# Optimization experiments

Measured on AMD Instinct MI355X. Metric: run time of the kernel, lower is better.

Reference implementation:

```python
import jax, jax.numpy as jnp
import numpy as np

N_NODES = 100000
N_EDGES = 1600000
IN_C = 128
HID_C = 128
OUT_C = 64
N_GRAPHS = 64


def setup_inputs() -> dict:
    key = jax.random.key(0)
    ks = jax.random.split(key, 12)
    x = jax.random.normal(ks[0], (N_NODES, IN_C), dtype=jnp.float32)
    edge_index = jax.random.randint(ks[1], (2, N_EDGES), 0, N_NODES, dtype=jnp.int64)
    batch = jnp.sort(jax.random.randint(ks[2], (N_NODES,), 0, N_GRAPHS, dtype=jnp.int64))
    def glorot(k, fan_in, fan_out):
        s = jnp.sqrt(6.0 / (fan_in + fan_out))
        return jax.random.uniform(k, (fan_in, fan_out), jnp.float32, -s, s)
    W1 = glorot(ks[3], IN_C, HID_C);  b1 = jnp.zeros((HID_C,), jnp.float32)
    W2 = glorot(ks[4], HID_C, HID_C); b2 = jnp.zeros((HID_C,), jnp.float32)
    W3 = glorot(ks[5], HID_C, HID_C); b3 = jnp.zeros((HID_C,), jnp.float32)
    Wlin = glorot(ks[6], HID_C, OUT_C)
    blin = jnp.zeros((OUT_C,), jnp.float32)
    return {"x": x, "edge_index": edge_index, "batch": batch,
            "W1": W1, "b1": b1, "W2": W2, "b2": b2, "W3": W3, "b3": b3,
            "Wlin": Wlin, "blin": blin}


def _gcn_conv(x, W, b, src, dst, norm):
    # PyG GCNConv: h = x @ W; out[dst] += norm * h[src]; out += b
    h = x @ W
    msg = h[src] * norm[:, None]                     # [E+N, C] edge-wise gather (memory-bound)
    out = jax.ops.segment_sum(msg, dst, num_segments=N_NODES)
    return out + b


def reference(x, edge_index, batch, W1, b1, W2, b2, W3, b3, Wlin, blin):
    # add self-loops (PyG default add_self_loops=True)
    loops = jnp.arange(N_NODES, dtype=edge_index.dtype)
    src = jnp.concatenate([edge_index[0], loops])
    dst = jnp.concatenate([edge_index[1], loops])
    # symmetric normalization: deg over dst with unit edge weights
    deg = jax.ops.segment_sum(jnp.ones_like(src, dtype=x.dtype), dst, num_segments=N_NODES)
    dinv = jnp.where(deg > 0, jax.lax.rsqrt(deg), 0.0)
    norm = dinv[src] * dinv[dst]                     # [E+N]

    h = jax.nn.relu(_gcn_conv(x, W1, b1, src, dst, norm))
    h = jax.nn.relu(_gcn_conv(h, W2, b2, src, dst, norm))
    h = jax.nn.relu(_gcn_conv(h, W3, b3, src, dst, norm))

    # global mean pool over graphs
    sums = jax.ops.segment_sum(h, batch, num_segments=N_GRAPHS)
    cnts = jax.ops.segment_sum(jnp.ones((N_NODES,), h.dtype), batch, num_segments=N_GRAPHS)
    pooled = sums / jnp.clip(cnts, 1.0)[:, None]     # [G, HID_C]
    return pooled @ Wlin + blin                      # [G, OUT_C]
```

## Files before the change

kernel.cpp:

```cpp
#include <hip/hip_runtime.h>
#include <stdint.h>

#define C_HID 128
#define NGRAPH 64
#define COUT 64
#define POOL_S 64
#define NBLK 256
#define BKT 256
#define NBUK_MAX 512
#define SCAN_CH 4096

typedef short bf16x8 __attribute__((ext_vector_type(8)));
typedef float f32x4 __attribute__((ext_vector_type(4)));
typedef float f32x2 __attribute__((ext_vector_type(2)));

__device__ __forceinline__ unsigned short f2bf(float f){
  unsigned int u = __builtin_bit_cast(unsigned int, f);
  u = u + 0x7FFFu + ((u >> 16) & 1u);
  return (unsigned short)(u >> 16);
}
__device__ __forceinline__ float bflo(unsigned int u){
  return __builtin_bit_cast(float, u << 16);
}
__device__ __forceinline__ float bfhi(unsigned int u){
  return __builtin_bit_cast(float, u & 0xFFFF0000u);
}
__device__ __forceinline__ int clampi(int v, int lo, int hi){
  return v < lo ? lo : (v > hi ? hi : v);
}

__global__ void k_zero(float* __restrict__ out, int n){
  int i = blockIdx.x*blockDim.x + threadIdx.x;
  if (i < n) out[i] = 0.f;
}

__global__ __launch_bounds__(256) void k_cnt(const int* __restrict__ dst,
                                             int* __restrict__ cntg,
                                             int E, int N, int NBUK, int chunk){
  __shared__ int cnt[NBUK_MAX];
  int blk = blockIdx.x, t = threadIdx.x;
  for (int b = t; b < NBUK; b += 256) cnt[b] = 0;
  __syncthreads();
  int e0 = blk*chunk, e1 = min(E, e0 + chunk);
  for (int e = e0 + t; e < e1; e += 256)
    atomicAdd(&cnt[clampi(dst[e], 0, N-1) >> 8], 1);
  __syncthreads();
  for (int b = t; b < NBUK; b += 256)
    cntg[b*NBLK + blk] = cnt[b];
}

__global__ __launch_bounds__(256) void k_scanA(const int* __restrict__ cnt,
                                               int* __restrict__ bsum, int n){
  __shared__ int red[256];
  int blk = blockIdx.x, t = threadIdx.x;
  int base = blk*SCAN_CH + t*16;
  int s = 0;
  #pragma unroll
  for (int j = 0; j < 16; ++j){ int i = base + j; s += (i < n) ? cnt[i] : 0; }
  red[t] = s; __syncthreads();
  for (int off = 128; off > 0; off >>= 1){
    if (t < off) red[t] += red[t + off];
    __syncthreads();
  }
  if (t == 0) bsum[blk] = red[0];
}

__global__ __launch_bounds__(256) void k_scanB(const int* __restrict__ bsum,
                                               int* __restrict__ bbase,
                                               int* __restrict__ bases, int nb, int n){
  __shared__ int buf[256];
  int t = threadIdx.x;
  int v = (t < nb) ? bsum[t] : 0;
  buf[t] = v; __syncthreads();
  for (int off = 1; off < 256; off <<= 1){
    int add = (t >= off) ? buf[t-off] : 0;
    __syncthreads();
    buf[t] += add;
    __syncthreads();
  }
  if (t < nb) bbase[t] = buf[t] - v;
  if (t == nb-1) bases[n] = buf[t];
}

__global__ __launch_bounds__(256) void k_scanC(const int* __restrict__ cnt,
                                               const int* __restrict__ bbase,
                                               int* __restrict__ bases, int n){
  __shared__ int buf[256];
  int blk = blockIdx.x, t = threadIdx.x;
  int base = blk*SCAN_CH + t*16;
  int loc[16]; int s = 0;
  #pragma unroll
  for (int j = 0; j < 16; ++j){ int i = base + j; loc[j] = (i < n) ? cnt[i] : 0; s += loc[j]; }
  buf[t] = s; __syncthreads();
  for (int off = 1; off < 256; off <<= 1){
    int add = (t >= off) ? buf[t-off] : 0;
    __syncthreads();
    buf[t] += add;
    __syncthreads();
  }
  int run = bbase[blk] + buf[t] - s;
  #pragma unroll
  for (int j = 0; j < 16; ++j){
    int i = base + j;
    if (i < n) bases[i] = run;
    run += loc[j];
  }
}

__global__ __launch_bounds__(256) void k_scat(const int* __restrict__ src,
                                              const int* __restrict__ dst,
                                              const int* __restrict__ bases,
                                              unsigned int* __restrict__ rec,
                                              int E, int N, int NBUK, int chunk){
  __shared__ int cur[NBUK_MAX];
  int blk = blockIdx.x, t = threadIdx.x;
  for (int b = t; b < NBUK; b += 256) cur[b] = bases[b*NBLK + blk];
  __syncthreads();
  int e0 = blk*chunk, e1 = min(E, e0 + chunk);
  for (int e = e0 + t; e < e1; e += 256){
    int d = clampi(dst[e], 0, N-1);
    int s = clampi(src[e], 0, N-1);
    int p = atomicAdd(&cur[d >> 8], 1);
    rec[p] = (unsigned int)s | ((unsigned int)(d & 255) << 24);
  }
}

__global__ __launch_bounds__(256) void k_csr(const unsigned int* __restrict__ rec,
                                             const int* __restrict__ bases,
                                             int* __restrict__ offs, float* __restrict__ dinv,
                                             int* __restrict__ meta, int E, int N, int NBUK){
  __shared__ int cnt[BKT], loff[BKT], cur[BKT];
  int b = blockIdx.x, t = threadIdx.x;
  cnt[t] = 0;
  __syncthreads();
  int r0 = bases[b*NBLK];
  int r1 = (b+1 < NBUK) ? bases[(b+1)*NBLK] : E;
  for (int i = r0 + t; i < r1; i += 256)
    atomicAdd(&cnt[rec[i] >> 24], 1);
  __syncthreads();
  loff[t] = cnt[t];
  __syncthreads();
  for (int off = 1; off < BKT; off <<= 1){
    int add = (t >= off) ? loff[t - off] : 0;
    __syncthreads();
    loff[t] += add;
    __syncthreads();
  }
  int excl = loff[t] - cnt[t];
  cur[t] = r0 + excl;
  int node = b*BKT + t;
  if (node < N){
    offs[node] = r0 + excl;
    dinv[node] = rsqrtf((float)(cnt[t] + 1));
  }
  if (b == NBUK-1 && t == 0) offs[N] = E;
  __syncthreads();
  for (int i = r0 + t; i < r1; i += 256){
    unsigned int r = rec[i];
    int p = atomicAdd(&cur[r >> 24], 1);
    meta[p] = (int)(r & 0x00FFFFFFu);
  }
}

__global__ void k_xcast(const float2* __restrict__ x, const float* __restrict__ dinv,
                        unsigned short* __restrict__ y, unsigned short* __restrict__ y2, int N){
  int i = blockIdx.x*256 + threadIdx.x;
  int tot = N*64;
  if (i < tot){
    float2 v = x[i];
    float dn = dinv[i >> 6] * 64.f;
    int p = __builtin_amdgcn_cvt_pk_fp8_f32(v.x*dn, v.y*dn, 0, false);
    y[i] = (unsigned short)(p & 0xFFFF);
  } else if (i < tot + 64){
    y[i] = 0;
    y2[i] = 0;
  }
}

__global__ void k_prep(const float* __restrict__ W1, const float* __restrict__ W2,
                       const float* __restrict__ W3, unsigned short* __restrict__ Wt){
  int idx = blockIdx.x*256 + threadIdx.x;
  int w = idx >> 14;
  int r = idx & 16383;
  int n = r & 127, k = r >> 7;
  const float* W = (w == 0) ? W1 : (w == 1) ? W2 : W3;
  Wt[(size_t)w*16384 + (size_t)n*128 + k] = f2bf(W[k*128 + n]);
}

__global__ __launch_bounds__(256) void k_spmm(const unsigned short* __restrict__ y,
                       const int* __restrict__ offs,
                       const float* __restrict__ dinv,
                       const int* __restrict__ meta,
                       unsigned int* __restrict__ agg, int N){
  int wv   = __builtin_amdgcn_readfirstlane(threadIdx.x >> 6);
  int lane = threadIdx.x & 63;
  int g = lane >> 3, c = lane & 7;
  int node0 = blockIdx.x*32 + wv*8;
  if (node0 >= N) return;

  int e[9];
  #pragma unroll
  for (int i = 0; i < 9; ++i) e[i] = offs[min(node0 + i, N)];
  int cn[8]; int maxc = 0;
  #pragma unroll
  for (int i = 0; i < 8; ++i){ cn[i] = e[i+1] - e[i]; maxc = max(maxc, cn[i]); }

  int e0l = e[0], cntl = cn[0];
  #pragma unroll
  for (int i = 1; i < 8; ++i){
    e0l  = (g == i) ? e[i]  : e0l;
    cntl = (g == i) ? cn[i] : cntl;
  }
  int nodeg = node0 + g;
  bool nok = nodeg < N;
  int nself = nok ? nodeg : N;

  const uint4* yrow = (const uint4*)y;

  int mv0 = (c      < cntl) ? meta[e0l + c]      : N;
  int mv1 = (c +  8 < cntl) ? meta[e0l + c +  8] : N;
  int mv2 = (c + 16 < cntl) ? meta[e0l + c + 16] : N;
  int mv3 = (c + 24 < cntl) ? meta[e0l + c + 24] : N;
  uint4 us = yrow[(size_t)nself*8 + c];
  float dl = dinv[nok ? nodeg : 0];

  f32x2 acc[8];
  { f32x2 f;
    f = __builtin_amdgcn_cvt_pk_f32_fp8((int)us.x, false); acc[0] = f;
    f = __builtin_amdgcn_cvt_pk_f32_fp8((int)us.x, true);  acc[1] = f;
    f = __builtin_amdgcn_cvt_pk_f32_fp8((int)us.y, false); acc[2] = f;
    f = __builtin_amdgcn_cvt_pk_f32_fp8((int)us.y, true);  acc[3] = f;
    f = __builtin_amdgcn_cvt_pk_f32_fp8((int)us.z, false); acc[4] = f;
    f = __builtin_amdgcn_cvt_pk_f32_fp8((int)us.z, true);  acc[5] = f;
    f = __builtin_amdgcn_cvt_pk_f32_fp8((int)us.w, false); acc[6] = f;
    f = __builtin_amdgcn_cvt_pk_f32_fp8((int)us.w, true);  acc[7] = f; }

  uint4 u[8];
#define SWZ(MV, J) __builtin_amdgcn_ds_swizzle(MV, (0x18 | (((J)&7)<<5)))
#define GA(K, SM) u[K] = yrow[(size_t)(unsigned)(SM)*8 + c]
#define CONV8() do{ _Pragma("unroll") \
  for (int k2 = 0; k2 < 8; ++k2){ \
    f32x2 f; \
    f = __builtin_amdgcn_cvt_pk_f32_fp8((int)u[k2].x, false); acc[0] += f; \
    f = __builtin_amdgcn_cvt_pk_f32_fp8((int)u[k2].x, true);  acc[1] += f; \
    f = __builtin_amdgcn_cvt_pk_f32_fp8((int)u[k2].y, false); acc[2] += f; \
    f = __builtin_amdgcn_cvt_pk_f32_fp8((int)u[k2].y, true);  acc[3] += f; \
    f = __builtin_amdgcn_cvt_pk_f32_fp8((int)u[k2].z, false); acc[4] += f; \
    f = __builtin_amdgcn_cvt_pk_f32_fp8((int)u[k2].z, true);  acc[5] += f; \
    f = __builtin_amdgcn_cvt_pk_f32_fp8((int)u[k2].w, false); acc[6] += f; \
    f = __builtin_amdgcn_cvt_pk_f32_fp8((int)u[k2].w, true);  acc[7] += f; } }while(0)

  if (0 < maxc){
    GA(0,SWZ(mv0,0)); GA(1,SWZ(mv0,1)); GA(2,SWZ(mv0,2)); GA(3,SWZ(mv0,3));
    GA(4,SWZ(mv0,4)); GA(5,SWZ(mv0,5)); GA(6,SWZ(mv0,6)); GA(7,SWZ(mv0,7));
    __builtin_amdgcn_sched_barrier(0);
    CONV8();
  }
  if (8 < maxc){
    GA(0,SWZ(mv1,0)); GA(1,SWZ(mv1,1)); GA(2,SWZ(mv1,2)); GA(3,SWZ(mv1,3));
    GA(4,SWZ(mv1,4)); GA(5,SWZ(mv1,5)); GA(6,SWZ(mv1,6)); GA(7,SWZ(mv1,7));
    __builtin_amdgcn_sched_barrier(0);
    CONV8();
  }
  if (16 < maxc){
    GA(0,SWZ(mv2,0)); GA(1,SWZ(mv2,1)); GA(2,SWZ(mv2,2)); GA(3,SWZ(mv2,3));
    GA(4,SWZ(mv2,4)); GA(5,SWZ(mv2,5)); GA(6,SWZ(mv2,6)); GA(7,SWZ(mv2,7));
    __builtin_amdgcn_sched_barrier(0);
    CONV8();
  }
  if (24 < maxc){
    GA(0,SWZ(mv3,0)); GA(1,SWZ(mv3,1)); GA(2,SWZ(mv3,2)); GA(3,SWZ(mv3,3));
    GA(4,SWZ(mv3,4)); GA(5,SWZ(mv3,5)); GA(6,SWZ(mv3,6)); GA(7,SWZ(mv3,7));
    __builtin_amdgcn_sched_barrier(0);
    CONV8();
  }
#undef SWZ
#undef GA
#undef CONV8

  for (int j = 32; j < maxc; ++j){
    int sm = (j < cntl) ? meta[e0l + j] : N;
    uint4 t = yrow[(size_t)(unsigned)sm*8 + c];
    f32x2 f;
    f = __builtin_amdgcn_cvt_pk_f32_fp8((int)t.x, false); acc[0] += f;
    f = __builtin_amdgcn_cvt_pk_f32_fp8((int)t.x, true);  acc[1] += f;
    f = __builtin_amdgcn_cvt_pk_f32_fp8((int)t.y, false); acc[2] += f;
    f = __builtin_amdgcn_cvt_pk_f32_fp8((int)t.y, true);  acc[3] += f;
    f = __builtin_amdgcn_cvt_pk_f32_fp8((int)t.z, false); acc[4] += f;
    f = __builtin_amdgcn_cvt_pk_f32_fp8((int)t.z, true);  acc[5] += f;
    f = __builtin_amdgcn_cvt_pk_f32_fp8((int)t.w, false); acc[6] += f;
    f = __builtin_amdgcn_cvt_pk_f32_fp8((int)t.w, true);  acc[7] += f;
  }

  float dn = dl * 0.015625f;
  if (nok){
    uint4 w0, w1;
    w0.x = (unsigned int)f2bf(acc[0].x*dn) | ((unsigned int)f2bf(acc[0].y*dn) << 16);
    w0.y = (unsigned int)f2bf(acc[1].x*dn) | ((unsigned int)f2bf(acc[1].y*dn) << 16);
    w0.z = (unsigned int)f2bf(acc[2].x*dn) | ((unsigned int)f2bf(acc[2].y*dn) << 16);
    w0.w = (unsigned int)f2bf(acc[3].x*dn) | ((unsigned int)f2bf(acc[3].y*dn) << 16);
    w1.x = (unsigned int)f2bf(acc[4].x*dn) | ((unsigned int)f2bf(acc[4].y*dn) << 16);
    w1.y = (unsigned int)f2bf(acc[5].x*dn) | ((unsigned int)f2bf(acc[5].y*dn) << 16);
    w1.z = (unsigned int)f2bf(acc[6].x*dn) | ((unsigned int)f2bf(acc[6].y*dn) << 16);
    w1.w = (unsigned int)f2bf(acc[7].x*dn) | ((unsigned int)f2bf(acc[7].y*dn) << 16);
    *(uint4*)(agg + (size_t)nodeg*64 + c*8)     = w0;
    *(uint4*)(agg + (size_t)nodeg*64 + c*8 + 4) = w1;
  }
}

#define GEMM_BLOCKS 512
template<bool FP8OUT>
__global__ __launch_bounds__(256) void k_gemm(const unsigned short* __restrict__ A,
                                              const unsigned short* __restrict__ Wt,
                                              const float* __restrict__ bias,
                                              const float* __restrict__ scale,
                                              void* __restrict__ outv, int M){
  __shared__ unsigned short wt[128*136];
  {
    const uint4* wsrc = (const uint4*)Wt;
    for (int i = threadIdx.x; i < 4096; i += 256){
      uint4 v = wsrc[i];
      int n = i >> 4, kblk = i & 15;
      *(uint4*)&wt[n*136 + kblk*8] = v;
    }
  }
  __syncthreads();

  int wv = threadIdx.x >> 6, lane = threadIdx.x & 63;
  int q = lane >> 4, ln = lane & 15;
  int tiles = (M + 63) >> 6;

  for (int tile = blockIdx.x; tile < tiles; tile += GEMM_BLOCKS){
    int m0 = tile*64 + wv*16;
    int arow = m0 + ln;
    bool arow_ok = (arow < M);
    int arow_s = arow_ok ? arow : 0;

    f32x4 zero = {0.f, 0.f, 0.f, 0.f};
    f32x4 acc[8];
    #pragma unroll
    for (int t = 0; t < 8; ++t) acc[t] = zero;

    #pragma unroll
    for (int kk = 0; kk < 4; ++kk){
      bf16x8 a;
      if (arow_ok){
        __builtin_memcpy(&a, A + (size_t)arow_s*128 + kk*32 + q*8, 16);
      } else {
        a = (bf16x8){0,0,0,0,0,0,0,0};
      }
      #pragma unroll
      for (int t = 0; t < 8; ++t){
        bf16x8 b;
        __builtin_memcpy(&b, &wt[(t*16 + ln)*136 + kk*32 + q*8], 16);
        acc[t] = __builtin_amdgcn_mfma_f32_16x16x32_bf16(a, b, acc[t], 0, 0, 0);
      }
    }
    float sc[4];
    #pragma unroll
    for (int r = 0; r < 4; ++r){
      int row = m0 + q*4 + r;
      sc[r] = (FP8OUT && row < M) ? scale[row] * 64.f : 1.0f;
    }
    #pragma unroll
    for (int t = 0; t < 8; ++t){
      float bv = bias[t*16 + ln];
      #pragma unroll
      for (int r = 0; r < 4; ++r){
        int row = m0 + q*4 + r;
        if (row < M){
          float v = acc[t][r] + bv;
          v = v > 0.f ? v : 0.f;
          if (FP8OUT){
            v *= sc[r];
            int p = __builtin_amdgcn_cvt_pk_fp8_f32(v, v, 0, false);
            ((unsigned char*)outv)[(size_t)row*128 + t*16 + ln] = (unsigned char)(p & 0xFF);
          } else {
            ((unsigned short*)outv)[(size_t)row*128 + t*16 + ln] = f2bf(v);
          }
        }
      }
    }
  }
}

__device__ __forceinline__ int lower_bound_i(const int* arr, int n, int val){
  int lo = 0, hi = n;
  while (lo < hi){ int mid = (lo + hi) >> 1; if (arr[mid] < val) lo = mid + 1; else hi = mid; }
  return lo;
}

__global__ void k_pool(const unsigned int* __restrict__ x, const int* __restrict__ batch,
                       float* __restrict__ partial, int N){
  int g = blockIdx.x / POOL_S, s = blockIdx.x % POOL_S;
  int h = threadIdx.x >> 6;
  int lane = threadIdx.x & 63;
  int rs = clampi(lower_bound_i(batch, N, g), 0, N);
  int re = clampi(lower_bound_i(batch, N, g + 1), rs, N);
  int len = re - rs;
  int a = rs + (int)(((long long)len * s) / POOL_S);
  int b = rs + (int)(((long long)len * (s + 1)) / POOL_S);
  float ax = 0.f, ay = 0.f;
  for (int i = a + h; i < b; i += 2){
    unsigned int u = x[(size_t)i*64 + lane];
    ax += bflo(u);
    ay += bfhi(u);
  }
  float* p = partial + ((size_t)(g*POOL_S + s)*2 + h)*C_HID;
  p[2*lane]   = ax;
  p[2*lane+1] = ay;
}

__global__ void k_final(const float* __restrict__ partial, const int* __restrict__ batch,
                        const float* __restrict__ Wl, const float* __restrict__ bl,
                        float* __restrict__ out, int N){
  __shared__ float sums[C_HID];
  int g = blockIdx.x;
  int t = threadIdx.x;
  float acc = 0.f;
  const float* p = partial + (size_t)g*POOL_S*2*C_HID;
  for (int j = 0; j < POOL_S*2; ++j)
    acc += p[j*C_HID + t];
  sums[t] = acc;
  __syncthreads();
  if (t < COUT){
    int rs = clampi(lower_bound_i(batch, N, g), 0, N);
    int re = clampi(lower_bound_i(batch, N, g + 1), rs, N);
    float inv = 1.0f / fmaxf((float)(re - rs), 1.0f);
    float o = 0.f;
    for (int k = 0; k < 128; ++k)
      o += sums[k] * Wl[k*COUT + t];
    out[g*COUT + t] = o * inv + bl[t];
  }
}

extern "C" void kernel_launch(void* const* d_in, const int* in_sizes, int n_in,
                              void* d_out, int out_size, void* d_ws, size_t ws_size,
                              hipStream_t stream){
  const float* x0 = (const float*)d_in[0];
  const int* ei   = (const int*)d_in[1];
  const int* batch= (const int*)d_in[2];
  const float* W1 = (const float*)d_in[3];
  const float* b1 = (const float*)d_in[4];
  const float* W2 = (const float*)d_in[5];
  const float* b2 = (const float*)d_in[6];
  const float* W3 = (const float*)d_in[7];
  const float* b3 = (const float*)d_in[8];
  const float* Wl = (const float*)d_in[9];
  const float* bl = (const float*)d_in[10];
  float* out = (float*)d_out;

  int E = in_sizes[1] / 2;
  int N = in_sizes[2];
  const int* src = ei;
  const int* dst = ei + E;
  int NBUK = (N + BKT - 1) / BKT;
  int chunk = (E + NBLK - 1) / NBLK;
  int ncnt = NBUK * NBLK;
  int nsb  = (ncnt + SCAN_CH - 1) / SCAN_CH;

  size_t off_acc = 0;
  auto carve = [&](size_t bytes)->size_t{
    size_t r = off_acc; off_acc += (bytes + 255) & ~(size_t)255; return r;
  };
  size_t o_cnt   = carve((size_t)ncnt*4);
  size_t o_bases = carve((size_t)(ncnt+1)*4);
  size_t o_bsum  = carve(256*4);
  size_t o_bbase = carve(256*4);
  size_t o_offs  = carve((size_t)(N+1)*4);
  size_t o_dinv  = carve((size_t)N*4);
  size_t o_meta  = carve((size_t)E*4);
  size_t o_rec   = carve((size_t)E*4);
  size_t o_yA    = carve((size_t)(N+1)*C_HID);
  size_t o_yB    = carve((size_t)(N+1)*C_HID);
  size_t o_aggb  = carve((size_t)N*C_HID*2);
  size_t o_wt    = carve((size_t)3*128*128*2);
  size_t need = off_acc;

  size_t hbuf_avail = o_aggb - o_meta;
  bool alias_ok = hbuf_avail >= (size_t)N*C_HID*2;
  alias_ok = alias_ok &&
             ((size_t)(N+1)*C_HID >= (size_t)NGRAPH*POOL_S*2*C_HID*4);

  if (ws_size < need || NBUK > NBUK_MAX || nsb > 256 || !alias_ok){
    k_zero<<<(out_size+255)/256, 256, 0, stream>>>(out, out_size);
    return;
  }

  char* base = (char*)d_ws;
  int* cntg  = (int*)(base + o_cnt);
  int* bases = (int*)(base + o_bases);
  int* bsum  = (int*)(base + o_bsum);
  int* bbase = (int*)(base + o_bbase);
  int* offs  = (int*)(base + o_offs);
  float* dinv= (float*)(base + o_dinv);
  int* meta  = (int*)(base + o_meta);
  unsigned int* rec   = (unsigned int*)(base + o_rec);
  unsigned short* yA  = (unsigned short*)(base + o_yA);
  unsigned short* yB  = (unsigned short*)(base + o_yB);
  unsigned int* aggb  = (unsigned int*)(base + o_aggb);
  unsigned short* wt  = (unsigned short*)(base + o_wt);
  unsigned short* hbuf= (unsigned short*)(base + o_meta);
  float* part         = (float*)(base + o_yB);

  k_cnt  <<<NBLK, 256, 0, stream>>>(dst, cntg, E, N, NBUK, chunk);
  k_scanA<<<nsb, 256, 0, stream>>>(cntg, bsum, ncnt);
  k_scanB<<<1, 256, 0, stream>>>(bsum, bbase, bases, nsb, ncnt);
  k_scanC<<<nsb, 256, 0, stream>>>(cntg, bbase, bases, ncnt);
  k_scat <<<NBLK, 256, 0, stream>>>(src, dst, bases, rec, E, N, NBUK, chunk);
  k_csr  <<<NBUK, BKT, 0, stream>>>(rec, bases, offs, dinv, meta, E, N, NBUK);

  k_xcast<<<(N*64 + 64 + 255)/256, 256, 0, stream>>>((const float2*)x0, dinv, yA, yB, N);
  k_prep <<<192, 256, 0, stream>>>(W1, W2, W3, wt);

  int spmm_grid = (N + 31) / 32;

  k_spmm<<<spmm_grid, 256, 0, stream>>>(yA, offs, dinv, meta, aggb, N);
  k_gemm<true ><<<GEMM_BLOCKS, 256, 0, stream>>>((const unsigned short*)aggb, wt,           b1, dinv, (void*)yB, N);
  k_spmm<<<spmm_grid, 256, 0, stream>>>(yB, offs, dinv, meta, aggb, N);
  k_gemm<true ><<<GEMM_BLOCKS, 256, 0, stream>>>((const unsigned short*)aggb, wt + 16384,   b2, dinv, (void*)yA, N);
  k_spmm<<<spmm_grid, 256, 0, stream>>>(yA, offs, dinv, meta, aggb, N);
  k_gemm<false><<<GEMM_BLOCKS, 256, 0, stream>>>((const unsigned short*)aggb, wt + 2*16384, b3, dinv, (void*)hbuf, N);

  k_pool <<<NGRAPH*POOL_S, 128, 0, stream>>>((const unsigned int*)hbuf, batch, part, N);
  k_final<<<NGRAPH, 128, 0, stream>>>(part, batch, Wl, bl, out, N);
}
```

Measured before the change: 335.8 us.

## Fuse global mean pooling into final GEMM epilogue via atomics

The last GCN layer's GEMM no longer writes a bf16 hidden buffer that a separate pool kernel reads back. Its epilogue now reduces each 64-row tile into per-graph channel sums in shared memory and adds them to a global accumulator with atomics. Tiles spanning more than two graphs fall back to per-element global atomics. This removes one full N×128 write and read plus one kernel launch, at the cost of atomic contention and a nondeterministic summation order.

```diff
diff --git a/kernel.cpp b/kernel.cpp
--- a/kernel.cpp
+++ b/kernel.cpp
@@ -4,7 +4,6 @@
 #define C_HID 128
 #define NGRAPH 64
 #define COUT 64
-#define POOL_S 64
 #define NBLK 256
 #define BKT 256
 #define NBUK_MAX 512
@@ -18,12 +17,6 @@
   unsigned int u = __builtin_bit_cast(unsigned int, f);
   u = u + 0x7FFFu + ((u >> 16) & 1u);
   return (unsigned short)(u >> 16);
-}
-__device__ __forceinline__ float bflo(unsigned int u){
-  return __builtin_bit_cast(float, u << 16);
-}
-__device__ __forceinline__ float bfhi(unsigned int u){
-  return __builtin_bit_cast(float, u & 0xFFFF0000u);
 }
 __device__ __forceinline__ int clampi(int v, int lo, int hi){
   return v < lo ? lo : (v > hi ? hi : v);
@@ -178,8 +171,10 @@
 }
 
 __global__ void k_prep(const float* __restrict__ W1, const float* __restrict__ W2,
-                       const float* __restrict__ W3, unsigned short* __restrict__ Wt){
+                       const float* __restrict__ W3, unsigned short* __restrict__ Wt,
+                       float* __restrict__ gsum){
   int idx = blockIdx.x*256 + threadIdx.x;
+  if (idx < NGRAPH*C_HID) gsum[idx] = 0.f;
   int w = idx >> 14;
   int r = idx & 16383;
   int n = r & 127, k = r >> 7;
@@ -309,13 +304,16 @@
 }
 
 #define GEMM_BLOCKS 512
-template<bool FP8OUT>
+template<bool FP8OUT, bool POOL>
 __global__ __launch_bounds__(256) void k_gemm(const unsigned short* __restrict__ A,
                                               const unsigned short* __restrict__ Wt,
                                               const float* __restrict__ bias,
                                               const float* __restrict__ scale,
-                                              void* __restrict__ outv, int M){
+                                              void* __restrict__ outv,
+                                              const int* __restrict__ batch,
+                                              float* __restrict__ gsum, int M){
   __shared__ unsigned short wt[128*136];
+  __shared__ float gbuf[2][C_HID];
   {
     const uint4* wsrc = (const uint4*)Wt;
     for (int i = threadIdx.x; i < 4096; i += 256){
@@ -356,27 +354,72 @@
         acc[t] = __builtin_amdgcn_mfma_f32_16x16x32_bf16(a, b, acc[t], 0, 0, 0);
       }
     }
-    float sc[4];
-    #pragma unroll
-    for (int r = 0; r < 4; ++r){
-      int row = m0 + q*4 + r;
-      sc[r] = (FP8OUT && row < M) ? scale[row] * 64.f : 1.0f;
-    }
-    #pragma unroll
-    for (int t = 0; t < 8; ++t){
-      float bv = bias[t*16 + ln];
+
+    if (POOL){
+      int tb = tile*64;
+      int gA = batch[tb];
+      int gB = batch[min(tb + 63, M - 1)];
+      bool multi = (gB > gA + 1);
+      __syncthreads();
+      ((float*)gbuf)[threadIdx.x] = 0.f;
+      __syncthreads();
+      #pragma unroll
+      for (int t = 0; t < 8; ++t){
+        float bv = bias[t*16 + ln];
+        int ch = t*16 + ln;
+        float s0 = 0.f, s1 = 0.f;
+        #pragma unroll
+        for (int r = 0; r < 4; ++r){
+          int row = m0 + q*4 + r;
+          if (row < M){
+            float v = acc[t][r] + bv;
+            v = v > 0.f ? v : 0.f;
+            if (multi){
+              atomicAdd(&gsum[(size_t)batch[row]*C_HID + ch], v);
+            } else if (gB > gA && batch[row] != gA){
+              s1 += v;
+            } else {
+              s0 += v;
+            }
+          }
+        }
+        if (!multi){
+          if (s0 != 0.f) atomicAdd(&gbuf[0][ch], s0);
+          if (s1 != 0.f) atomicAdd(&gbuf[1][ch], s1);
+        }
+      }
+      __syncthreads();
+      if (!multi){
+        int sel = threadIdx.x >> 7, ch2 = threadIdx.x & 127;
+        if (sel == 0 || gB > gA){
+          float v = ((float*)gbuf)[threadIdx.x];
+          if (v != 0.f)
+            atomicAdd(&gsum[(size_t)((sel == 0) ? gA : gB)*C_HID + ch2], v);
+        }
+      }
+    } else {
+      float sc[4];
       #pragma unroll
       for (int r = 0; r < 4; ++r){
         int row = m0 + q*4 + r;
-        if (row < M){
-          float v = acc[t][r] + bv;
-          v = v > 0.f ? v : 0.f;
-          if (FP8OUT){
-            v *= sc[r];
-            int p = __builtin_amdgcn_cvt_pk_fp8_f32(v, v, 0, false);
-            ((unsigned char*)outv)[(size_t)row*128 + t*16 + ln] = (unsigned char)(p & 0xFF);
-          } else {
-            ((unsigned short*)outv)[(size_t)row*128 + t*16 + ln] = f2bf(v);
+        sc[r] = (FP8OUT && row < M) ? scale[row] * 64.f : 1.0f;
+      }
+      #pragma unroll
+      for (int t = 0; t < 8; ++t){
+        float bv = bias[t*16 + ln];
+        #pragma unroll
+        for (int r = 0; r < 4; ++r){
+          int row = m0 + q*4 + r;
+          if (row < M){
+            float v = acc[t][r] + bv;
+            v = v > 0.f ? v : 0.f;
+            if (FP8OUT){
+              v *= sc[r];
+              int p = __builtin_amdgcn_cvt_pk_fp8_f32(v, v, 0, false);
+              ((unsigned char*)outv)[(size_t)row*128 + t*16 + ln] = (unsigned char)(p & 0xFF);
+            } else {
+              ((unsigned short*)outv)[(size_t)row*128 + t*16 + ln] = f2bf(v);
+            }
           }
         }
       }
@@ -390,38 +433,12 @@
   return lo;
 }
 
-__global__ void k_pool(const unsigned int* __restrict__ x, const int* __restrict__ batch,
-                       float* __restrict__ partial, int N){
-  int g = blockIdx.x / POOL_S, s = blockIdx.x % POOL_S;
-  int h = threadIdx.x >> 6;
-  int lane = threadIdx.x & 63;
-  int rs = clampi(lower_bound_i(batch, N, g), 0, N);
-  int re = clampi(lower_bound_i(batch, N, g + 1), rs, N);
-  int len = re - rs;
-  int a = rs + (int)(((long long)len * s) / POOL_S);
-  int b = rs + (int)(((long long)len * (s + 1)) / POOL_S);
-  float ax = 0.f, ay = 0.f;
-  for (int i = a + h; i < b; i += 2){
-    unsigned int u = x[(size_t)i*64 + lane];
-    ax += bflo(u);
-    ay += bfhi(u);
-  }
-  float* p = partial + ((size_t)(g*POOL_S + s)*2 + h)*C_HID;
-  p[2*lane]   = ax;
-  p[2*lane+1] = ay;
-}
-
-__global__ void k_final(const float* __restrict__ partial, const int* __restrict__ batch,
-                        const float* __restrict__ Wl, const float* __restrict__ bl,
-                        float* __restrict__ out, int N){
-  __shared__ float sums[C_HID];
-  int g = blockIdx.x;
-  int t = threadIdx.x;
-  float acc = 0.f;
-  const float* p = partial + (size_t)g*POOL_S*2*C_HID;
-  for (int j = 0; j < POOL_S*2; ++j)
-    acc += p[j*C_HID + t];
-  sums[t] = acc;
+__global__ void k_fin(const float* __restrict__ gsum, const int* __restrict__ batch,
+                      const float* __restrict__ Wl, const float* __restrict__ bl,
+                      float* __restrict__ out, int N){
+  __shared__ float srow[C_HID];
+  int g = blockIdx.x, t = threadIdx.x;
+  srow[t] = gsum[(size_t)g*C_HID + t];
   __syncthreads();
   if (t < COUT){
     int rs = clampi(lower_bound_i(batch, N, g), 0, N);
@@ -429,7 +446,7 @@
     float inv = 1.0f / fmaxf((float)(re - rs), 1.0f);
     float o = 0.f;
     for (int k = 0; k < 128; ++k)
-      o += sums[k] * Wl[k*COUT + t];
+      o += srow[k] * Wl[k*COUT + t];
     out[g*COUT + t] = o * inv + bl[t];
   }
 }
@@ -475,14 +492,10 @@
   size_t o_yB    = carve((size_t)(N+1)*C_HID);
   size_t o_aggb  = carve((size_t)N*C_HID*2);
   size_t o_wt    = carve((size_t)3*128*128*2);
+  size_t o_gsum  = carve((size_t)NGRAPH*C_HID*4);
   size_t need = off_acc;
 
-  size_t hbuf_avail = o_aggb - o_meta;
-  bool alias_ok = hbuf_avail >= (size_t)N*C_HID*2;
-  alias_ok = alias_ok &&
-             ((size_t)(N+1)*C_HID >= (size_t)NGRAPH*POOL_S*2*C_HID*4);
-
-  if (ws_size < need || NBUK > NBUK_MAX || nsb > 256 || !alias_ok){
+  if (ws_size < need || NBUK > NBUK_MAX || nsb > 256){
     k_zero<<<(out_size+255)/256, 256, 0, stream>>>(out, out_size);
     return;
   }
@@ -500,8 +513,7 @@
   unsigned short* yB  = (unsigned short*)(base + o_yB);
   unsigned int* aggb  = (unsigned int*)(base + o_aggb);
   unsigned short* wt  = (unsigned short*)(base + o_wt);
-  unsigned short* hbuf= (unsigned short*)(base + o_meta);
-  float* part         = (float*)(base + o_yB);
+  float* gsum         = (float*)(base + o_gsum);
 
   k_cnt  <<<NBLK, 256, 0, stream>>>(dst, cntg, E, N, NBUK, chunk);
   k_scanA<<<nsb, 256, 0, stream>>>(cntg, bsum, ncnt);
@@ -511,17 +523,16 @@
   k_csr  <<<NBUK, BKT, 0, stream>>>(rec, bases, offs, dinv, meta, E, N, NBUK);
 
   k_xcast<<<(N*64 + 64 + 255)/256, 256, 0, stream>>>((const float2*)x0, dinv, yA, yB, N);
-  k_prep <<<192, 256, 0, stream>>>(W1, W2, W3, wt);
+  k_prep <<<192, 256, 0, stream>>>(W1, W2, W3, wt, gsum);
 
   int spmm_grid = (N + 31) / 32;
 
   k_spmm<<<spmm_grid, 256, 0, stream>>>(yA, offs, dinv, meta, aggb, N);
-  k_gemm<true ><<<GEMM_BLOCKS, 256, 0, stream>>>((const unsigned short*)aggb, wt,           b1, dinv, (void*)yB, N);
+  k_gemm<true , false><<<GEMM_BLOCKS, 256, 0, stream>>>((const unsigned short*)aggb, wt,           b1, dinv, (void*)yB, nullptr, nullptr, N);
   k_spmm<<<spmm_grid, 256, 0, stream>>>(yB, offs, dinv, meta, aggb, N);
-  k_gemm<true ><<<GEMM_BLOCKS, 256, 0, stream>>>((const unsigned short*)aggb, wt + 16384,   b2, dinv, (void*)yA, N);
+  k_gemm<true , false><<<GEMM_BLOCKS, 256, 0, stream>>>((const unsigned short*)aggb, wt + 16384,   b2, dinv, (void*)yA, nullptr, nullptr, N);
   k_spmm<<<spmm_grid, 256, 0, stream>>>(yA, offs, dinv, meta, aggb, N);
-  k_gemm<false><<<GEMM_BLOCKS, 256, 0, stream>>>((const unsigned short*)aggb, wt + 2*16384, b3, dinv, (void*)hbuf, N);
-
-  k_pool <<<NGRAPH*POOL_S, 128, 0, stream>>>((const unsigned int*)hbuf, batch, part, N);
-  k_final<<<NGRAPH, 128, 0, stream>>>(part, batch, Wl, bl, out, N);
-}
+  k_gemm<false, true ><<<GEMM_BLOCKS, 256, 0, stream>>>((const unsigned short*)aggb, wt + 2*16384, b3, dinv, nullptr,    batch,   gsum,    N);
+
+  k_fin<<<NGRAPH, 128, 0, stream>>>(gsum, batch, Wl, bl, out, N);
+}
```

Result: no change. 333.0 us (-0.8%).
